# Optimization experiments

Hardware: AMD Instinct MI355X
Metric: run time of the kernel (lower is better)

## Reference

```python
import jax, jax.numpy as jnp
import numpy as np

P = 7      # local_patch_size
H = 6      # heads
DH = 30    # dim_head


def setup_inputs() -> dict:
    key = jax.random.key(0)
    ks = jax.random.split(key, 5)
    b, dim, L = 16, 180, 14336
    inner = H * DH  # 180
    fmap = jax.random.normal(ks[0], (b, dim, L), dtype=jnp.float32)
    Wq = jax.random.normal(ks[1], (inner, dim), dtype=jnp.float32) * 0.05
    Wkv = jax.random.normal(ks[2], (2 * inner, dim), dtype=jnp.float32) * 0.05
    Wo = jax.random.normal(ks[3], (dim, inner), dtype=jnp.float32) * 0.05
    bo = jax.random.normal(ks[4], (dim,), dtype=jnp.float32) * 0.05
    return {"fmap": fmap, "Wq": Wq, "Wkv": Wkv, "Wo": Wo, "bo": bo}


def reference(fmap, Wq, Wkv, Wo, bo):
    b, c, L = fmap.shape
    l = L // P
    scale = DH ** -0.5
    # 'b c (l p) -> b c l p' windows
    x = fmap.reshape(b, c, l, P)
    # pointwise (kernel-1) conv projections
    q = jnp.einsum('ec,bclp->belp', Wq, x)
    kv = jnp.einsum('ec,bclp->belp', Wkv, x)
    k, v = jnp.split(kv, 2, axis=1)

    def split_heads(t):
        # (b, h*d, l, p) -> (b, l, h, p, d)
        return t.reshape(b, H, DH, l, P).transpose(0, 3, 1, 4, 2)

    q, k, v = map(split_heads, (q, k, v))
    dots = jnp.einsum('blhid,blhjd->blhij', q, k) * scale  # per-window 7x7 scores
    attn = jax.nn.softmax(dots, axis=-1)
    out = jnp.einsum('blhij,blhjd->blhid', attn, v)  # (b, l, h, p, d)
    # '(b l h) p d -> b (h d) (l p)'
    out = out.transpose(0, 2, 4, 1, 3).reshape(b, H * DH, l * P)
    return jnp.einsum('oe,bel->bol', Wo, out) + bo[None, :, None]
```

## Files before the change

### kernel.cpp

```cpp
#include <hip/hip_runtime.h>
#include <stdint.h>

namespace {

constexpr int DIM  = 180;
constexpr int LL   = 14336;
constexpr int B    = 16;
constexpr int T    = 56;
constexpr int NCH  = 256;
constexpr int EQKV = 540;

constexpr int QTS = 552;
constexpr int XSS = 200;

typedef __attribute__((ext_vector_type(8))) short bf16x8;
typedef __attribute__((ext_vector_type(4))) float f32x4;

__device__ __forceinline__ unsigned short f2b(float f) {
  uint32_t u = __builtin_bit_cast(uint32_t, f);
  u = (u + 0x7fffu + ((u >> 16) & 1u)) >> 16;
  return (unsigned short)u;
}
__device__ __forceinline__ uint32_t pack2(float lo, float hi) {
  return (uint32_t)f2b(lo) | ((uint32_t)f2b(hi) << 16);
}
__device__ __forceinline__ float blo(uint32_t u) { return __builtin_bit_cast(float, u << 16); }
__device__ __forceinline__ float bhi(uint32_t u) { return __builtin_bit_cast(float, u & 0xffff0000u); }
__device__ __forceinline__ f32x4 zero4() { f32x4 z = {0.f,0.f,0.f,0.f}; return z; }

}

__global__ __launch_bounds__(1024) void la_prep(
    const float* __restrict__ Wq, const float* __restrict__ Wkv,
    const float* __restrict__ Wo, unsigned short* __restrict__ wqkv_b,
    unsigned short* __restrict__ wo_b) {
  const int idx = (int)(blockIdx.x * 1024 + threadIdx.x);
  if (idx < 576 * 192) {
    const int e = idx / 192, c = idx - e * 192;
    float v = 0.f;
    if (e < EQKV && c < DIM)
      v = (e < DIM) ? Wq[e * DIM + c] : Wkv[(size_t)(e - DIM) * DIM + c];
    wqkv_b[idx] = f2b(v);
  } else {
    const int k = idx - 576 * 192;
    if (k < 192 * 192) {
      const int o = k / 192, c = k - o * 192;
      float v = 0.f;
      if (o < DIM && c < DIM) v = Wo[o * DIM + c];
      wo_b[k] = f2b(v);
    }
  }
}

__global__ __launch_bounds__(512, 4) void la_main(
    const float* __restrict__ fmap, const unsigned short* __restrict__ wqkv,
    const unsigned short* __restrict__ wo_b, const float* __restrict__ bo,
    float* __restrict__ out) {
  __shared__ __align__(16) unsigned short qt[T * QTS];
  __shared__ __align__(16) unsigned short xs[32 * XSS];

  const int tid  = (int)threadIdx.x;
  const int wave = tid >> 6;
  const int lane = tid & 63;
  const int l15  = lane & 15;
  const int g    = lane >> 4;

  const int bi    = (int)blockIdx.x;
  const int b     = bi >> 8;
  const int chunk = bi & 255;
  const int t0    = chunk * T;

  const unsigned short* wA = wqkv + (size_t)l15 * 192 + g * 8;

#pragma unroll
  for (int ph = 0; ph < 2; ++ph) {
    const int tb = ph * 32;
#pragma unroll
    for (int it = 0; it < 3; ++it) {
      const int idx = tid + it * 512;
      const int c  = idx >> 3;
      const int tq = (idx & 7) * 4;
      float4 v = {0.f, 0.f, 0.f, 0.f};
      if (c < DIM && (tb + tq) < T)
        v = *(const float4*)(fmap + (size_t)(b * DIM + c) * LL + t0 + tb + tq);
      unsigned short* xr = xs + tq * XSS + c;
      xr[0 * XSS] = f2b(v.x);
      xr[1 * XSS] = f2b(v.y);
      xr[2 * XSS] = f2b(v.z);
      xr[3 * XSS] = f2b(v.w);
    }
    bf16x8 An[6];
#pragma unroll
    for (int ks = 0; ks < 6; ++ks)
      An[ks] = *(const bf16x8*)(wA + (size_t)(wave * 16) * 192 + ks * 32);
    __syncthreads();
    bf16x8 b0[6], b1[6];
#pragma unroll
    for (int ks = 0; ks < 6; ++ks) {
      b0[ks] = *(const bf16x8*)(xs + l15 * XSS + ks * 32 + g * 8);
      b1[ks] = *(const bf16x8*)(xs + (16 + l15) * XSS + ks * 32 + g * 8);
    }
    int mt = wave;
#pragma unroll 5
    for (int it = 0; it < 5; ++it) {
      if (mt < 36) {
        bf16x8 A[6];
#pragma unroll
        for (int ks = 0; ks < 6; ++ks) A[ks] = An[ks];
        const int mtn = mt + 8;
        if (mtn < 36) {
#pragma unroll
          for (int ks = 0; ks < 6; ++ks)
            An[ks] = *(const bf16x8*)(wA + (size_t)(mtn * 16) * 192 + ks * 32);
        }
        f32x4 a0 = zero4(), a1 = zero4();
#pragma unroll
        for (int ks = 0; ks < 6; ++ks) {
          a0 = __builtin_amdgcn_mfma_f32_16x16x32_bf16(A[ks], b0[ks], a0, 0, 0, 0);
          a1 = __builtin_amdgcn_mfma_f32_16x16x32_bf16(A[ks], b1[ks], a1, 0, 0, 0);
        }
        const int e0 = mt * 16 + g * 4;
        if (e0 < EQKV) {
          const int ta = tb + l15;
          uint2 pk;
          pk.x = pack2(a0[0], a0[1]);
          pk.y = pack2(a0[2], a0[3]);
          *(uint2*)(qt + ta * QTS + e0) = pk;
          const int tb2 = tb + 16 + l15;
          if (tb2 < T) {
            uint2 pk2;
            pk2.x = pack2(a1[0], a1[1]);
            pk2.y = pack2(a1[2], a1[3]);
            *(uint2*)(qt + tb2 * QTS + e0) = pk2;
          }
        }
      }
      mt += 8;
    }
    __syncthreads();
  }

  const float scale = 0.18257418583505536f;
#pragma unroll
  for (int rnd = 0; rnd < 2; ++rnd) {
    const int task = tid + rnd * 512;
    if (task < 672) {
      const int pair = task >> 1;
      const int half = task & 1;
      const int w    = pair / 42;
      const int rem  = pair - w * 42;
      const int h    = rem / 7;
      const int i    = rem - h * 7;
      const int ti   = w * 7 + i;
      const int hq   = 30 * h;
      const unsigned short* qp = qt + ti * QTS + hq;
      const unsigned short* kb = qt + (w * 7) * QTS + DIM + hq;
      const unsigned short* vb = qt + (w * 7) * QTS + 2 * DIM + hq;
      float dots[7];
#pragma unroll
      for (int j = 0; j < 7; ++j) dots[j] = 0.f;
#pragma unroll
      for (int dq = 0; dq < 8; ++dq) {
        const int dp = half + 2 * dq;
        if (dp < 15) {
          const uint32_t qu = *(const uint32_t*)(qp + 2 * dp);
          const float q0 = blo(qu), q1 = bhi(qu);
#pragma unroll
          for (int j = 0; j < 7; ++j) {
            const uint32_t ku = *(const uint32_t*)(kb + j * QTS + 2 * dp);
            dots[j] += q0 * blo(ku);
            dots[j] += q1 * bhi(ku);
          }
        }
      }
#pragma unroll
      for (int j = 0; j < 7; ++j) dots[j] += __shfl_xor(dots[j], 1);
      float mx = dots[0];
#pragma unroll
      for (int j = 1; j < 7; ++j) mx = fmaxf(mx, dots[j]);
      float aw[7];
      float s = 0.f;
#pragma unroll
      for (int j = 0; j < 7; ++j) {
        const float pj = __expf(scale * (dots[j] - mx));
        aw[j] = pj; s += pj;
      }
      const float inv = 1.f / s;
#pragma unroll
      for (int j = 0; j < 7; ++j) aw[j] *= inv;
      uint32_t* orow = (uint32_t*)(qt + ti * QTS + hq);
#pragma unroll
      for (int dq = 0; dq < 8; ++dq) {
        const int dp = half + 2 * dq;
        if (dp < 15) {
          float o0 = 0.f, o1 = 0.f;
#pragma unroll
          for (int j = 0; j < 7; ++j) {
            const uint32_t vu = *(const uint32_t*)(vb + j * QTS + 2 * dp);
            o0 += aw[j] * blo(vu);
            o1 += aw[j] * bhi(vu);
          }
          orow[dp] = pack2(o0, o1);
        }
      }
    }
  }
  __syncthreads();

  {
    const int n3 = wave & 3;
    const int m3 = (wave >> 2) * 6;
    const int tc  = n3 * 16 + l15;
    const int trd = (tc < T) ? tc : (T - 1);
    bf16x8 bq[6];
#pragma unroll
    for (int ks = 0; ks < 6; ++ks)
      bq[ks] = *(const bf16x8*)(qt + trd * QTS + ks * 32 + g * 8);
    const unsigned short* wO = wo_b + (size_t)l15 * 192 + g * 8;
    bf16x8 An[6];
#pragma unroll
    for (int ks = 0; ks < 6; ++ks)
      An[ks] = *(const bf16x8*)(wO + (size_t)(m3 * 16) * 192 + ks * 32);
#pragma unroll 6
    for (int k6 = 0; k6 < 6; ++k6) {
      const int m = m3 + k6;
      bf16x8 A[6];
#pragma unroll
      for (int ks = 0; ks < 6; ++ks) A[ks] = An[ks];
      if (k6 < 5) {
#pragma unroll
        for (int ks = 0; ks < 6; ++ks)
          An[ks] = *(const bf16x8*)(wO + (size_t)((m + 1) * 16) * 192 + ks * 32);
      }
      f32x4 acc = zero4();
#pragma unroll
      for (int ks = 0; ks < 6; ++ks)
        acc = __builtin_amdgcn_mfma_f32_16x16x32_bf16(A[ks], bq[ks], acc, 0, 0, 0);
      if (tc < T) {
#pragma unroll
        for (int r = 0; r < 4; ++r) {
          const int o = m * 16 + g * 4 + r;
          if (o < DIM)
            out[(size_t)(b * DIM + o) * LL + t0 + tc] = acc[r] + bo[o];
        }
      }
    }
  }
}

extern "C" void kernel_launch(void* const* d_in, const int* in_sizes, int n_in,
                              void* d_out, int out_size, void* d_ws, size_t ws_size,
                              hipStream_t stream) {
  const float* fmap = (const float*)d_in[0];
  const float* Wq   = (const float*)d_in[1];
  const float* Wkv  = (const float*)d_in[2];
  const float* Wo   = (const float*)d_in[3];
  const float* bo   = (const float*)d_in[4];
  float* o = (float*)d_out;

  unsigned short* wqkv_b = (unsigned short*)d_ws;
  unsigned short* wo_b   = wqkv_b + 576 * 192;

  const int prep_elems = 576 * 192 + 192 * 192;
  hipLaunchKernelGGL(la_prep, dim3((prep_elems + 1023) / 1024), dim3(1024), 0,
                     stream, Wq, Wkv, Wo, wqkv_b, wo_b);
  hipLaunchKernelGGL(la_main, dim3(B * NCH), dim3(512), 0, stream,
                     fmap, wqkv_b, wo_b, bo, o);
}
```

Measured before the change: 432.3 us.

## Compute windowed attention with MFMA using head-padded Q/K layout and transposed V

Replaces the scalar per-thread 7x7 window attention with MFMA 16x16x32 ops. Each tile covers two windows (14 tokens) of one head and masks scores across windows. Q and K are stored with heads padded to 32 columns, V goes into a separate transposed LDS buffer, and Wo is re-laid out to match the padded head columns. The aim is to cut LDS traffic and VALU work in the attention phase. The cost is extra LDS, wasted MFMA lanes on padding and masks, and scattered scalar stores for V that may cause bank conflicts.

```diff
diff --git a/kernel.cpp b/kernel.cpp
--- a/kernel.cpp
+++ b/kernel.cpp
@@ -10,11 +10,18 @@
 constexpr int NCH  = 256;
 constexpr int EQKV = 540;
 
-constexpr int QTS = 552;
-constexpr int XSS = 200;
+constexpr int QTS  = 392;
+constexpr int KOFF = 192;
+constexpr int QT_U16  = T * QTS;
+constexpr int VT_U16  = 24 * 512;
+constexpr int XSS     = 200;
+constexpr int XS_U16  = 32 * XSS;
+constexpr int LDS_U16 = QT_U16 + VT_U16 + XS_U16;
 
 typedef __attribute__((ext_vector_type(8))) short bf16x8;
 typedef __attribute__((ext_vector_type(4))) float f32x4;
+
+union Frag { bf16x8 v; uint32_t u[4]; unsigned short s[8]; };
 
 __device__ __forceinline__ unsigned short f2b(float f) {
   uint32_t u = __builtin_bit_cast(uint32_t, f);
@@ -24,8 +31,6 @@
 __device__ __forceinline__ uint32_t pack2(float lo, float hi) {
   return (uint32_t)f2b(lo) | ((uint32_t)f2b(hi) << 16);
 }
-__device__ __forceinline__ float blo(uint32_t u) { return __builtin_bit_cast(float, u << 16); }
-__device__ __forceinline__ float bhi(uint32_t u) { return __builtin_bit_cast(float, u & 0xffff0000u); }
 __device__ __forceinline__ f32x4 zero4() { f32x4 z = {0.f,0.f,0.f,0.f}; return z; }
 
 }
@@ -33,7 +38,7 @@
 __global__ __launch_bounds__(1024) void la_prep(
     const float* __restrict__ Wq, const float* __restrict__ Wkv,
     const float* __restrict__ Wo, unsigned short* __restrict__ wqkv_b,
-    unsigned short* __restrict__ wo_b) {
+    unsigned short* __restrict__ wo_h) {
   const int idx = (int)(blockIdx.x * 1024 + threadIdx.x);
   if (idx < 576 * 192) {
     const int e = idx / 192, c = idx - e * 192;
@@ -44,20 +49,23 @@
   } else {
     const int k = idx - 576 * 192;
     if (k < 192 * 192) {
-      const int o = k / 192, c = k - o * 192;
+      const int o = k / 192, cc = k - o * 192;
+      const int h = cc >> 5, d = cc & 31;
       float v = 0.f;
-      if (o < DIM && c < DIM) v = Wo[o * DIM + c];
-      wo_b[k] = f2b(v);
+      if (o < DIM && d < 30) v = Wo[o * DIM + h * 30 + d];
+      wo_h[k] = f2b(v);
     }
   }
 }
 
 __global__ __launch_bounds__(512, 4) void la_main(
     const float* __restrict__ fmap, const unsigned short* __restrict__ wqkv,
-    const unsigned short* __restrict__ wo_b, const float* __restrict__ bo,
+    const unsigned short* __restrict__ wo_h, const float* __restrict__ bo,
     float* __restrict__ out) {
-  __shared__ __align__(16) unsigned short qt[T * QTS];
-  __shared__ __align__(16) unsigned short xs[32 * XSS];
+  __shared__ __align__(16) unsigned short lds[LDS_U16];
+  unsigned short* qt = lds;
+  unsigned short* vt = lds + QT_U16;
+  unsigned short* xs = lds + QT_U16 + VT_U16;
 
   const int tid  = (int)threadIdx.x;
   const int wave = tid >> 6;
@@ -71,6 +79,10 @@
   const int t0    = chunk * T;
 
   const unsigned short* wA = wqkv + (size_t)l15 * 192 + g * 8;
+
+#pragma unroll
+  for (int it = 0; it < 3; ++it)
+    ((uint4*)vt)[tid + it * 512] = make_uint4(0u, 0u, 0u, 0u);
 
 #pragma unroll
   for (int ph = 0; ph < 2; ++ph) {
@@ -121,17 +133,31 @@
         }
         const int e0 = mt * 16 + g * 4;
         if (e0 < EQKV) {
-          const int ta = tb + l15;
-          uint2 pk;
-          pk.x = pack2(a0[0], a0[1]);
-          pk.y = pack2(a0[2], a0[3]);
-          *(uint2*)(qt + ta * QTS + e0) = pk;
-          const int tb2 = tb + 16 + l15;
-          if (tb2 < T) {
-            uint2 pk2;
-            pk2.x = pack2(a1[0], a1[1]);
-            pk2.y = pack2(a1[2], a1[3]);
-            *(uint2*)(qt + tb2 * QTS + e0) = pk2;
+#pragma unroll
+          for (int nt = 0; nt < 2; ++nt) {
+            const f32x4 A4 = nt ? a1 : a0;
+            const int t = tb + nt * 16 + l15;
+            if (t < T) {
+              if (e0 < 360) {
+                unsigned short* qrow = qt + t * QTS;
+#pragma unroll
+                for (int pr = 0; pr < 2; ++pr) {
+                  const int e = e0 + 2 * pr;
+                  int col;
+                  if (e < 180) { const int h = e / 30; col = e + 2 * h; }
+                  else { const int rr = e - 180; const int h = rr / 30; col = KOFF + rr + 2 * h; }
+                  *(uint32_t*)(qrow + col) = pack2(A4[2 * pr], A4[2 * pr + 1]);
+                }
+              } else {
+                const int wp = t / 14, jp = t - wp * 14;
+#pragma unroll
+                for (int r = 0; r < 4; ++r) {
+                  const int rr = e0 - 360 + r;
+                  const int h = rr / 30, d = rr - 30 * h;
+                  vt[((wp * 6 + h) << 9) + (d << 4) + jp] = f2b(A4[r]);
+                }
+              }
+            }
           }
         }
       }
@@ -142,66 +168,60 @@
 
   const float scale = 0.18257418583505536f;
 #pragma unroll
-  for (int rnd = 0; rnd < 2; ++rnd) {
-    const int task = tid + rnd * 512;
-    if (task < 672) {
-      const int pair = task >> 1;
-      const int half = task & 1;
-      const int w    = pair / 42;
-      const int rem  = pair - w * 42;
-      const int h    = rem / 7;
-      const int i    = rem - h * 7;
-      const int ti   = w * 7 + i;
-      const int hq   = 30 * h;
-      const unsigned short* qp = qt + ti * QTS + hq;
-      const unsigned short* kb = qt + (w * 7) * QTS + DIM + hq;
-      const unsigned short* vb = qt + (w * 7) * QTS + 2 * DIM + hq;
-      float dots[7];
-#pragma unroll
-      for (int j = 0; j < 7; ++j) dots[j] = 0.f;
-#pragma unroll
-      for (int dq = 0; dq < 8; ++dq) {
-        const int dp = half + 2 * dq;
-        if (dp < 15) {
-          const uint32_t qu = *(const uint32_t*)(qp + 2 * dp);
-          const float q0 = blo(qu), q1 = bhi(qu);
-#pragma unroll
-          for (int j = 0; j < 7; ++j) {
-            const uint32_t ku = *(const uint32_t*)(kb + j * QTS + 2 * dp);
-            dots[j] += q0 * blo(ku);
-            dots[j] += q1 * bhi(ku);
-          }
-        }
-      }
-#pragma unroll
-      for (int j = 0; j < 7; ++j) dots[j] += __shfl_xor(dots[j], 1);
-      float mx = dots[0];
-#pragma unroll
-      for (int j = 1; j < 7; ++j) mx = fmaxf(mx, dots[j]);
-      float aw[7];
-      float s = 0.f;
-#pragma unroll
-      for (int j = 0; j < 7; ++j) {
-        const float pj = __expf(scale * (dots[j] - mx));
-        aw[j] = pj; s += pj;
-      }
-      const float inv = 1.f / s;
-#pragma unroll
-      for (int j = 0; j < 7; ++j) aw[j] *= inv;
-      uint32_t* orow = (uint32_t*)(qt + ti * QTS + hq);
-#pragma unroll
-      for (int dq = 0; dq < 8; ++dq) {
-        const int dp = half + 2 * dq;
-        if (dp < 15) {
-          float o0 = 0.f, o1 = 0.f;
-#pragma unroll
-          for (int j = 0; j < 7; ++j) {
-            const uint32_t vu = *(const uint32_t*)(vb + j * QTS + 2 * dp);
-            o0 += aw[j] * blo(vu);
-            o1 += aw[j] * bhi(vu);
-          }
-          orow[dp] = pack2(o0, o1);
-        }
+  for (int u = 0; u < 3; ++u) {
+    const int unit = wave * 3 + u;
+    const int wp = unit / 6, h = unit - wp * 6;
+    const int twb = wp * 14;
+    const int arow = twb + l15;
+    const unsigned short* rowp = qt + ((arow < T) ? arow : (T - 1)) * QTS;
+    Frag A, Bq;
+    A.v  = *(const bf16x8*)(rowp + KOFF + (h << 5) + (g << 3));
+    Bq.v = *(const bf16x8*)(rowp + (h << 5) + (g << 3));
+    if (g == 3) { A.u[3] = 0; Bq.u[3] = 0; }
+    const f32x4 s = __builtin_amdgcn_mfma_f32_16x16x32_bf16(A.v, Bq.v, zero4(), 0, 0, 0);
+    float p[4];
+    float mx = -3e38f;
+#pragma unroll
+    for (int r = 0; r < 4; ++r) {
+      const int j = (g << 2) + r;
+      const bool valid = (l15 < 7) ? (j < 7) : (j >= 7 && j < 14);
+      p[r] = valid ? s[r] : -3e38f;
+      mx = fmaxf(mx, p[r]);
+    }
+    mx = fmaxf(mx, __shfl_xor(mx, 16));
+    mx = fmaxf(mx, __shfl_xor(mx, 32));
+    float sum = 0.f;
+#pragma unroll
+    for (int r = 0; r < 4; ++r) {
+      p[r] = __expf(scale * (p[r] - mx));
+      sum += p[r];
+    }
+    sum += __shfl_xor(sum, 16);
+    sum += __shfl_xor(sum, 32);
+    const float inv = 1.f / sum;
+#pragma unroll
+    for (int r = 0; r < 4; ++r) p[r] *= inv;
+    const uint32_t pk0 = pack2(p[0], p[1]);
+    const uint32_t pk1 = pack2(p[2], p[3]);
+    const int s0 = l15 + ((g & 1) << 5);
+    Frag PA;
+    PA.u[0] = __shfl(pk0, s0);
+    PA.u[1] = __shfl(pk1, s0);
+    PA.u[2] = __shfl(pk0, s0 + 16);
+    PA.u[3] = __shfl(pk1, s0 + 16);
+    if (g >= 2) { PA.u[0] = 0; PA.u[1] = 0; PA.u[2] = 0; PA.u[3] = 0; }
+    const unsigned short* vtb = vt + ((wp * 6 + h) << 9);
+    const bf16x8 V0 = *(const bf16x8*)(vtb + (l15 << 4) + (g << 3));
+    const bf16x8 V1 = *(const bf16x8*)(vtb + ((16 + l15) << 4) + (g << 3));
+    const f32x4 o0 = __builtin_amdgcn_mfma_f32_16x16x32_bf16(PA.v, V0, zero4(), 0, 0, 0);
+    const f32x4 o1 = __builtin_amdgcn_mfma_f32_16x16x32_bf16(PA.v, V1, zero4(), 0, 0, 0);
+#pragma unroll
+    for (int r = 0; r < 4; ++r) {
+      const int irow = (g << 2) + r;
+      if (irow < 14) {
+        unsigned short* orow = qt + (twb + irow) * QTS + (h << 5);
+        orow[l15] = f2b(o0[r]);
+        orow[16 + l15] = f2b(o1[r]);
       }
     }
   }
@@ -216,7 +236,7 @@
 #pragma unroll
     for (int ks = 0; ks < 6; ++ks)
       bq[ks] = *(const bf16x8*)(qt + trd * QTS + ks * 32 + g * 8);
-    const unsigned short* wO = wo_b + (size_t)l15 * 192 + g * 8;
+    const unsigned short* wO = wo_h + (size_t)l15 * 192 + g * 8;
     bf16x8 An[6];
 #pragma unroll
     for (int ks = 0; ks < 6; ++ks)
@@ -259,11 +279,11 @@
   float* o = (float*)d_out;
 
   unsigned short* wqkv_b = (unsigned short*)d_ws;
-  unsigned short* wo_b   = wqkv_b + 576 * 192;
+  unsigned short* wo_h   = wqkv_b + 576 * 192;
 
   const int prep_elems = 576 * 192 + 192 * 192;
   hipLaunchKernelGGL(la_prep, dim3((prep_elems + 1023) / 1024), dim3(1024), 0,
-                     stream, Wq, Wkv, Wo, wqkv_b, wo_b);
+                     stream, Wq, Wkv, Wo, wqkv_b, wo_h);
   hipLaunchKernelGGL(la_main, dim3(B * NCH), dim3(512), 0, stream,
-                     fmap, wqkv_b, wo_b, bo, o);
-}
+                     fmap, wqkv_b, wo_h, bo, o);
+}
```

Result: slower. 448.9 us (+3.8%).
